# Kernel optimization log

Hardware: AMD Instinct MI355X
Metric: run time of the kernel (lower is better)

Reference implementation:

```python
import jax, jax.numpy as jnp
import numpy as np
import math

B, S, D = 2, 4096, 512
H = 8
DH = D // H  # 64


def setup_inputs() -> dict:
    key = jax.random.key(0)
    k1, k2, k3, k4, k5 = jax.random.split(key, 5)
    scale = 1.0 / math.sqrt(D)
    return {
        "x": jax.random.normal(k1, (B, S, D), dtype=jnp.float32),
        "W_in": jax.random.normal(k2, (D, 3 * D), dtype=jnp.float32) * scale,
        "b_in": jax.random.normal(k3, (3 * D,), dtype=jnp.float32) * 0.01,
        "W_out": jax.random.normal(k4, (D, D), dtype=jnp.float32) * scale,
        "b_out": jax.random.normal(k5, (D,), dtype=jnp.float32) * 0.01,
        "causal_mask": 1,
    }


def reference(x, W_in, b_in, W_out, b_out, causal_mask):
    b, s, d = x.shape
    # fused QKV projection: (b, s, 3d)
    qkv = x @ W_in + b_in
    q, k, v = jnp.split(qkv, 3, axis=-1)
    # (b, s, d) -> (b, h, s, dh)
    def to_heads(t):
        return t.reshape(b, s, H, DH).transpose(0, 2, 1, 3)
    q, k, v = to_heads(q), to_heads(k), to_heads(v)
    # raw scores (b, h, s, s)
    scores = jnp.einsum("bhqd,bhkd->bhqk", q, k)
    if causal_mask:  # static python flag
        # upper-triangular (strictly above diag) -> -inf, applied pre-scaling
        # (matches source; -inf invariant under /sqrt(d_head))
        tri = jnp.triu(jnp.ones((s, s), dtype=bool), k=1)
        scores = jnp.where(tri, -jnp.inf, scores)
    attn = jax.nn.softmax(scores / math.sqrt(DH), axis=-1)
    out = jnp.einsum("bhqk,bhkd->bhqd", attn, v)
    out = out.transpose(0, 2, 1, 3).reshape(b, s, d)
    return out @ W_out + b_out
```

## Files before the change

### kernel.cpp

```cpp
#include <hip/hip_runtime.h>
#include <cstdint>
#include <cmath>

typedef unsigned short BF16;
typedef __attribute__((ext_vector_type(8))) short short8;
typedef __attribute__((ext_vector_type(4))) float f32x4;
typedef __attribute__((ext_vector_type(16))) float f32x16;
typedef __attribute__((ext_vector_type(2))) unsigned int uint2v;
typedef __attribute__((ext_vector_type(4))) unsigned int uint4v;

#define S_LEN 4096
#define DMODEL 512
#define NHEAD 8
#define DHEAD 64
#define BS 2
#define NROWS (BS * NHEAD * S_LEN)

__device__ __forceinline__ BF16 f2bf(float f) {
  union { float f; uint32_t u; } v; v.f = f;
  uint32_t r = (v.u + 0x7FFFu + ((v.u >> 16) & 1u)) >> 16;
  return (BF16)r;
}

__device__ __forceinline__ unsigned cvtpk(float a, float b) {
  unsigned r;
  asm volatile("v_cvt_pk_bf16_f32 %0, %1, %2" : "=v"(r) : "v"(a), "v"(b));
  return r;
}

__device__ __forceinline__ float partner32(float x, int hi) {
  unsigned a = __float_as_uint(x), b = a;
  uint2v r = __builtin_amdgcn_permlane32_swap(a, b, false, false);
  return __uint_as_float(hi ? r[0] : r[1]);
}

__device__ __forceinline__ void pl32(unsigned &a, unsigned &b) {
  uint2v r = __builtin_amdgcn_permlane32_swap(a, b, false, false);
  a = r[0]; b = r[1];
}

__device__ __forceinline__ void gload16(const void* g, void* lds) {
  __builtin_amdgcn_global_load_lds(
      (const __attribute__((address_space(1))) void*)g,
      (__attribute__((address_space(3))) void*)lds, 16, 0, 0);
}

#define MAX3(a, b, c) fmaxf(fmaxf((a), (b)), (c))
#define CS_CONST 0.18033688011112042f

__global__ __launch_bounds__(256) void cvt_x_k(const float* __restrict__ x,
                                               BF16* __restrict__ xb) {
  int i = blockIdx.x * 256 + threadIdx.x;
  float4 v = reinterpret_cast<const float4*>(x)[i];
  ushort4 o;
  o.x = f2bf(v.x); o.y = f2bf(v.y); o.z = f2bf(v.z); o.w = f2bf(v.w);
  reinterpret_cast<ushort4*>(xb)[i] = o;
}

__global__ __launch_bounds__(256) void tr_cvt_k(const float* __restrict__ W,
                                                BF16* __restrict__ Wt,
                                                int K, int N) {
  __shared__ float t[32][33];
  int n0 = blockIdx.x * 32, k0 = blockIdx.y * 32;
  int tx = threadIdx.x & 31, ty = threadIdx.x >> 5;
#pragma unroll
  for (int i = 0; i < 4; ++i)
    t[ty + 8 * i][tx] = W[(size_t)(k0 + ty + 8 * i) * N + n0 + tx];
  __syncthreads();
#pragma unroll
  for (int i = 0; i < 4; ++i)
    Wt[(size_t)(n0 + ty + 8 * i) * K + k0 + tx] = f2bf(t[tx][ty + 8 * i]);
}

template <int MODE>
__global__ __launch_bounds__(256)
void gemm_k(const BF16* __restrict__ A, const BF16* __restrict__ Bt,
            const float* __restrict__ bias,
            BF16* __restrict__ Qb, BF16* __restrict__ Kb, BF16* __restrict__ Vt,
            float* __restrict__ Out) {
  __shared__ BF16 As[128 * 64];
  __shared__ BF16 Bs[128 * 64];
  const int tid = threadIdx.x;
  const int l = tid & 63, w = tid >> 6;
  const int wm = w >> 1, wn = w & 1;
  const int bm = blockIdx.x, bn = blockIdx.y;
  f32x4 acc[4][4] = {};

  for (int kt = 0; kt < 512 / 64; ++kt) {
#pragma unroll
    for (int i = 0; i < 4; ++i) {
      int ldsoff = i * 4096 + w * 1024;
      int off = ldsoff + l * 16;
      int row = off >> 7;
      int slot = ((off >> 4) & 7) ^ (row & 7);
      gload16(A + (size_t)(bm * 128 + row) * 512 + kt * 64 + slot * 8,
              (char*)As + ldsoff);
      gload16(Bt + (size_t)(bn * 128 + row) * 512 + kt * 64 + slot * 8,
              (char*)Bs + ldsoff);
    }
    __syncthreads();
    const char* Ab = (const char*)As;
    const char* Bb = (const char*)Bs;
    short8 af[4][2], bfr[4][2];
#pragma unroll
    for (int mf = 0; mf < 4; ++mf)
#pragma unroll
      for (int kk = 0; kk < 2; ++kk) {
        int row = wm * 64 + mf * 16 + (l & 15);
        int slot = ((l >> 4) + 4 * kk) ^ (row & 7);
        af[mf][kk] = *(const short8*)(Ab + row * 128 + slot * 16);
      }
#pragma unroll
    for (int nf = 0; nf < 4; ++nf)
#pragma unroll
      for (int kk = 0; kk < 2; ++kk) {
        int row = wn * 64 + nf * 16 + (l & 15);
        int slot = ((l >> 4) + 4 * kk) ^ (row & 7);
        bfr[nf][kk] = *(const short8*)(Bb + row * 128 + slot * 16);
      }
    __builtin_amdgcn_s_setprio(1);
#pragma unroll
    for (int kk = 0; kk < 2; ++kk)
#pragma unroll
      for (int mf = 0; mf < 4; ++mf)
#pragma unroll
        for (int nf = 0; nf < 4; ++nf)
          acc[mf][nf] = __builtin_amdgcn_mfma_f32_16x16x32_bf16(
              af[mf][kk], bfr[nf][kk], acc[mf][nf], 0, 0, 0);
    __builtin_amdgcn_s_setprio(0);
    __syncthreads();
  }

#pragma unroll
  for (int mf = 0; mf < 4; ++mf)
#pragma unroll
    for (int nf = 0; nf < 4; ++nf)
#pragma unroll
      for (int r = 0; r < 4; ++r) {
        int row = bm * 128 + wm * 64 + mf * 16 + ((l >> 4) << 2) + r;
        int col = bn * 128 + wn * 64 + nf * 16 + (l & 15);
        float v = acc[mf][nf][r] + bias[col];
        if (MODE == 0) {
          int sec = col >> 9, nl = col & 511;
          int h = nl >> 6, dh = nl & 63;
          int b = row >> 12, s = row & 4095;
          size_t bh = (size_t)(b * NHEAD + h);
          if (sec == 0)
            Qb[(bh * S_LEN + s) * DHEAD + dh] = f2bf(v);
          else if (sec == 1)
            Kb[(bh * S_LEN + s) * DHEAD + dh] = f2bf(v);
          else
            Vt[(bh * DHEAD + dh) * S_LEN + s] = f2bf(v);
        } else {
          Out[(size_t)row * DMODEL + col] = v;
        }
      }
}

__global__ __launch_bounds__(256, 4)
void attn_k(const BF16* __restrict__ Qg, const BF16* __restrict__ Kg,
            const BF16* __restrict__ Vg, BF16* __restrict__ Opb,
            float* __restrict__ Ml) {
  __shared__ BF16 Kl[2][64 * 64];
  __shared__ BF16 Vl[2][64 * 64];
  const int tid = threadIdx.x, l = tid & 63, w = tid >> 6;
  const int hi = l >> 5, ln = l & 31;
  const int wgid = blockIdx.x;
  const int xcd = wgid & 7, j = wgid >> 3;
  const int bh = xcd * 2 + (j & 1);
  const int qr = (j >> 1) & 3;
  const int p = j >> 3;
  const BF16* Qh = Qg + (size_t)bh * S_LEN * DHEAD;
  const BF16* Kh = Kg + (size_t)bh * S_LEN * DHEAD;
  const BF16* Vh = Vg + (size_t)bh * DHEAD * S_LEN;
  const float CS = CS_CONST;

  int cur = 0;
  for (int rep = 0; rep < 2; ++rep) {
    const int qt = rep ? (31 - p) : p;
    const int qq = rep ? (3 - qr) : qr;
    const int NTf = 2 * qt + 2;
    const int kbase = (qq * NTf) >> 2;
    const int kend = ((qq + 1) * NTf) >> 2;
    const int NT = kend - kbase;
    const int q0w = qt * 128 + w * 32;
    const int qrow = q0w + ln;
    __syncthreads();

    short8 qb[4];
    {
      const BF16* qp = Qh + (size_t)qrow * DHEAD + hi * 8;
#pragma unroll
      for (int ks = 0; ks < 4; ++ks) qb[ks] = *(const short8*)(qp + ks * 16);
    }
    f32x16 oacc0 = {}, oacc1 = {};
    float m_ = -INFINITY, l_ = 0.f;

    auto stage = [&](int buf, int ktile) {
      const int kv0 = ktile * 64;
#pragma unroll
      for (int i = 0; i < 2; ++i) {
        int base = i * 4096 + w * 1024;
        int off = base + l * 16;
        int row = off >> 7;
        int slot = ((off >> 4) & 7) ^ (row & 7);
        gload16(Kh + (size_t)(kv0 + row) * DHEAD + slot * 8, (char*)Kl[buf] + base);
        gload16(Vh + (size_t)row * S_LEN + kv0 + slot * 8, (char*)Vl[buf] + base);
      }
    };

    if (NT > 0) {
      stage(cur, kbase);
      for (int kt = 0; kt < NT; ++kt) {
        __syncthreads();
        if (kt + 1 < NT) stage(cur ^ 1, kbase + kt + 1);
        const int kv0 = (kbase + kt) * 64;
        if (kv0 <= q0w + 31) {
          const char* Kb_ = (const char*)Kl[cur];
          f32x16 s0 = {}, s1 = {};
          __builtin_amdgcn_s_setprio(1);
#pragma unroll
          for (int ks = 0; ks < 4; ++ks) {
            int slot0 = (2 * ks + hi) ^ (ln & 7);
            short8 kf0 = *(const short8*)(Kb_ + ln * 128 + slot0 * 16);
            int row1 = 32 + ln;
            int slot1 = (2 * ks + hi) ^ (row1 & 7);
            short8 kf1 = *(const short8*)(Kb_ + row1 * 128 + slot1 * 16);
            s0 = __builtin_amdgcn_mfma_f32_32x32x16_bf16(kf0, qb[ks], s0, 0, 0, 0);
            s1 = __builtin_amdgcn_mfma_f32_32x32x16_bf16(kf1, qb[ks], s1, 0, 0, 0);
          }
          __builtin_amdgcn_s_setprio(0);
          if (kv0 + 63 > q0w) {
#pragma unroll
            for (int r = 0; r < 16; ++r) {
              int crow = (r & 3) + 8 * (r >> 2) + 4 * hi;
              if (kv0 + crow > qrow) s0[r] = -INFINITY;
              if (kv0 + 32 + crow > qrow) s1[r] = -INFINITY;
            }
          }
          float a0 = MAX3(s0[0], s0[1], s0[2]);
          float a1 = MAX3(s0[3], s0[4], s0[5]);
          float a2 = MAX3(s0[6], s0[7], s0[8]);
          float a3 = MAX3(s0[9], s0[10], s0[11]);
          float a4 = MAX3(s0[12], s0[13], s0[14]);
          float a5 = MAX3(s0[15], s1[0], s1[1]);
          float a6 = MAX3(s1[2], s1[3], s1[4]);
          float a7 = MAX3(s1[5], s1[6], s1[7]);
          float a8 = MAX3(s1[8], s1[9], s1[10]);
          float a9 = MAX3(s1[11], s1[12], s1[13]);
          float a10 = fmaxf(s1[14], s1[15]);
          float b0 = MAX3(a0, a1, a2);
          float b1 = MAX3(a3, a4, a5);
          float b2 = MAX3(a6, a7, a8);
          float b3 = fmaxf(a9, a10);
          float pmax = fmaxf(fmaxf(b0, b1), fmaxf(b2, b3));
          pmax = fmaxf(pmax, partner32(pmax, hi));
          bool need = (pmax - m_) * CS > 8.0f;
          if (__any(need)) {
            float mn = fmaxf(m_, pmax);
            float alpha = exp2f((m_ - mn) * CS);
            m_ = mn;
            l_ *= alpha;
#pragma unroll
            for (int r = 0; r < 16; ++r) { oacc0[r] *= alpha; oacc1[r] *= alpha; }
          }
          const float mb = m_ * CS;
          float p0[16], p1[16];
          float rs = 0.f;
#pragma unroll
          for (int r = 0; r < 16; ++r) { p0[r] = exp2f(fmaf(s0[r], CS, -mb)); rs += p0[r]; }
#pragma unroll
          for (int r = 0; r < 16; ++r) { p1[r] = exp2f(fmaf(s1[r], CS, -mb)); rs += p1[r]; }
          rs += partner32(rs, hi);
          l_ += rs;
          short8 pf[4];
#pragma unroll
          for (int hf = 0; hf < 2; ++hf) {
            const float* pp = hf ? p1 : p0;
            unsigned w01 = cvtpk(pp[0], pp[1]), w23 = cvtpk(pp[2], pp[3]);
            unsigned w45 = cvtpk(pp[4], pp[5]), w67 = cvtpk(pp[6], pp[7]);
            unsigned w89 = cvtpk(pp[8], pp[9]), wab = cvtpk(pp[10], pp[11]);
            unsigned wcd = cvtpk(pp[12], pp[13]), wef = cvtpk(pp[14], pp[15]);
            pl32(w01, w45);
            pl32(w23, w67);
            pl32(w89, wcd);
            pl32(wab, wef);
            union { uint4v u; short8 s; } c0, c1;
            c0.u = (uint4v){w01, w23, w45, w67};
            c1.u = (uint4v){w89, wab, wcd, wef};
            pf[hf * 2 + 0] = c0.s;
            pf[hf * 2 + 1] = c1.s;
          }
          const char* Vb_ = (const char*)Vl[cur];
          __builtin_amdgcn_s_setprio(1);
#pragma unroll
          for (int ks = 0; ks < 4; ++ks) {
            int slot0 = (2 * ks + hi) ^ (ln & 7);
            short8 vf0 = *(const short8*)(Vb_ + ln * 128 + slot0 * 16);
            int row1 = 32 + ln;
            int slot1 = (2 * ks + hi) ^ (row1 & 7);
            short8 vf1 = *(const short8*)(Vb_ + row1 * 128 + slot1 * 16);
            oacc0 = __builtin_amdgcn_mfma_f32_32x32x16_bf16(vf0, pf[ks], oacc0, 0, 0, 0);
            oacc1 = __builtin_amdgcn_mfma_f32_32x32x16_bf16(vf1, pf[ks], oacc1, 0, 0, 0);
          }
          __builtin_amdgcn_s_setprio(0);
        }
        cur ^= 1;
      }
    }

    BF16* Op = Opb + ((size_t)qq * NROWS + (size_t)bh * S_LEN + qrow) * DHEAD;
#pragma unroll
    for (int blk = 0; blk < 2; ++blk) {
      const f32x16 oa = blk ? oacc1 : oacc0;
#pragma unroll
      for (int g = 0; g < 4; ++g) {
        int dh0 = 8 * g + 4 * hi + 32 * blk;
        unsigned lo = cvtpk(oa[4 * g + 0], oa[4 * g + 1]);
        unsigned h2 = cvtpk(oa[4 * g + 2], oa[4 * g + 3]);
        uint2v st = {lo, h2};
        *(uint2v*)(Op + dh0) = st;
      }
    }
    if (hi == 0) {
      float2 ml = {m_, l_};
      *(float2*)(Ml + ((size_t)qq * NROWS + (size_t)bh * S_LEN + qrow) * 2) = ml;
    }
  }
}

__global__ __launch_bounds__(256)
void merge_k(const BF16* __restrict__ Opb, const float* __restrict__ Ml,
             BF16* __restrict__ Ob) {
  const int wv = blockIdx.x * 4 + (threadIdx.x >> 6);
  const int lane = threadIdx.x & 63;
  const int row0 = wv * 64;
  for (int r = 0; r < 64; ++r) {
    int row = row0 + r;
    float2 ml0 = *(const float2*)(Ml + (size_t)row * 2);
    float2 ml1 = *(const float2*)(Ml + ((size_t)NROWS + row) * 2);
    float2 ml2 = *(const float2*)(Ml + ((size_t)2 * NROWS + row) * 2);
    float2 ml3 = *(const float2*)(Ml + ((size_t)3 * NROWS + row) * 2);
    float m = fmaxf(fmaxf(ml0.x, ml1.x), fmaxf(ml2.x, ml3.x));
    float a0 = exp2f((ml0.x - m) * CS_CONST);
    float a1 = exp2f((ml1.x - m) * CS_CONST);
    float a2 = exp2f((ml2.x - m) * CS_CONST);
    float a3 = exp2f((ml3.x - m) * CS_CONST);
    float linv = 1.0f / (ml0.y * a0 + ml1.y * a1 + ml2.y * a2 + ml3.y * a3);
    union { unsigned short u; } t;
    auto ld = [&](int slot) -> float {
      unsigned short u = Opb[((size_t)slot * NROWS + row) * DHEAD + lane];
      unsigned x = ((unsigned)u) << 16;
      return __uint_as_float(x);
    };
    float o = (ld(0) * a0 + ld(1) * a1 + ld(2) * a2 + ld(3) * a3) * linv;
    (void)t;
    int bh = row >> 12, s = row & 4095;
    Ob[((size_t)((bh >> 3) * S_LEN + s)) * DMODEL + (bh & 7) * DHEAD + lane] = f2bf(o);
  }
}

extern "C" void kernel_launch(void* const* d_in, const int* in_sizes, int n_in,
                              void* d_out, int out_size, void* d_ws, size_t ws_size,
                              hipStream_t stream) {
  const float* x = (const float*)d_in[0];
  const float* W_in = (const float*)d_in[1];
  const float* b_in = (const float*)d_in[2];
  const float* W_out = (const float*)d_in[3];
  const float* b_out = (const float*)d_in[4];
  float* out = (float*)d_out;

  char* ws = (char*)d_ws;
  const size_t SZ_X = (size_t)BS * S_LEN * DMODEL * 2;
  const size_t SZ_OP = (size_t)NROWS * DHEAD * 2;
  BF16* xb    = (BF16*)(ws);
  BF16* wint  = (BF16*)(ws + SZ_X);
  BF16* woutt = (BF16*)(ws + SZ_X + 3 * DMODEL * DMODEL * 2);
  BF16* Qb    = (BF16*)(ws + SZ_X + 4 * DMODEL * DMODEL * 2);
  BF16* Kb    = (BF16*)((char*)Qb + SZ_X);
  BF16* Vt    = (BF16*)((char*)Kb + SZ_X);
  BF16* Ob    = (BF16*)((char*)Vt + SZ_X);
  BF16* Opb   = (BF16*)((char*)Ob + SZ_X);
  float* Ml   = (float*)((char*)Opb + 4 * SZ_OP);

  cvt_x_k<<<dim3((BS * S_LEN * DMODEL) / 4 / 256), 256, 0, stream>>>(x, xb);
  tr_cvt_k<<<dim3(3 * DMODEL / 32, DMODEL / 32), 256, 0, stream>>>(W_in, wint, DMODEL, 3 * DMODEL);
  tr_cvt_k<<<dim3(DMODEL / 32, DMODEL / 32), 256, 0, stream>>>(W_out, woutt, DMODEL, DMODEL);
  gemm_k<0><<<dim3(BS * S_LEN / 128, 3 * DMODEL / 128), 256, 0, stream>>>(
      xb, wint, b_in, Qb, Kb, Vt, nullptr);
  attn_k<<<dim3(1024), 256, 0, stream>>>(Qb, Kb, Vt, Opb, Ml);
  merge_k<<<dim3(256), 256, 0, stream>>>(Opb, Ml, Ob);
  gemm_k<1><<<dim3(BS * S_LEN / 128, DMODEL / 128), 256, 0, stream>>>(
      Ob, woutt, b_out, nullptr, nullptr, nullptr, out);
}
```

Before: 215.1 us.

## Merge weight transposes, add separate V transpose, MFMA row sums, vectorize merge

Several unrelated changes. The two weight-transpose launches become one kernel. The QKV GEMM now writes V in the same row-major layout as Q and K, and a new LDS-tiled kernel transposes it into the reused x buffer, which avoids the strided scattered V stores. Inside attention, the softmax row-sum reduction and its cross-lane permute are replaced by an extra MFMA against a ones vector, trading VALU work for matrix-core work. The merge kernel is vectorized to 8 bf16 per lane with packed stores and twice as many blocks. The extra launch and the third MFMA per step are the costs.

```diff
diff --git a/kernel.cpp b/kernel.cpp
--- a/kernel.cpp
+++ b/kernel.cpp
@@ -20,6 +20,10 @@
   union { float f; uint32_t u; } v; v.f = f;
   uint32_t r = (v.u + 0x7FFFu + ((v.u >> 16) & 1u)) >> 16;
   return (BF16)r;
+}
+
+__device__ __forceinline__ float bf2f(short u) {
+  return __uint_as_float(((unsigned)(unsigned short)u) << 16);
 }
 
 __device__ __forceinline__ unsigned cvtpk(float a, float b) {
@@ -57,11 +61,18 @@
   reinterpret_cast<ushort4*>(xb)[i] = o;
 }
 
-__global__ __launch_bounds__(256) void tr_cvt_k(const float* __restrict__ W,
-                                                BF16* __restrict__ Wt,
-                                                int K, int N) {
+__global__ __launch_bounds__(256) void trw_k(const float* __restrict__ W_in,
+                                             const float* __restrict__ W_out,
+                                             BF16* __restrict__ wint,
+                                             BF16* __restrict__ woutt) {
   __shared__ float t[32][33];
-  int n0 = blockIdx.x * 32, k0 = blockIdx.y * 32;
+  const bool second = blockIdx.x >= 48;
+  const float* W = second ? W_out : W_in;
+  BF16* Wt = second ? woutt : wint;
+  const int N = second ? DMODEL : 3 * DMODEL;
+  const int K = DMODEL;
+  int n0 = (second ? ((int)blockIdx.x - 48) : (int)blockIdx.x) * 32;
+  int k0 = blockIdx.y * 32;
   int tx = threadIdx.x & 31, ty = threadIdx.x >> 5;
 #pragma unroll
   for (int i = 0; i < 4; ++i)
@@ -76,7 +87,7 @@
 __global__ __launch_bounds__(256)
 void gemm_k(const BF16* __restrict__ A, const BF16* __restrict__ Bt,
             const float* __restrict__ bias,
-            BF16* __restrict__ Qb, BF16* __restrict__ Kb, BF16* __restrict__ Vt,
+            BF16* __restrict__ Qb, BF16* __restrict__ Kb, BF16* __restrict__ Vc,
             float* __restrict__ Out) {
   __shared__ BF16 As[128 * 64];
   __shared__ BF16 Bs[128 * 64];
@@ -144,17 +155,36 @@
           int sec = col >> 9, nl = col & 511;
           int h = nl >> 6, dh = nl & 63;
           int b = row >> 12, s = row & 4095;
-          size_t bh = (size_t)(b * NHEAD + h);
-          if (sec == 0)
-            Qb[(bh * S_LEN + s) * DHEAD + dh] = f2bf(v);
-          else if (sec == 1)
-            Kb[(bh * S_LEN + s) * DHEAD + dh] = f2bf(v);
-          else
-            Vt[(bh * DHEAD + dh) * S_LEN + s] = f2bf(v);
+          BF16* dst = sec == 0 ? Qb : (sec == 1 ? Kb : Vc);
+          dst[(((size_t)(b * NHEAD + h)) * S_LEN + s) * DHEAD + dh] = f2bf(v);
         } else {
           Out[(size_t)row * DMODEL + col] = v;
         }
       }
+}
+
+__global__ __launch_bounds__(256)
+void v_tr_k(const BF16* __restrict__ Vc, BF16* __restrict__ Vt) {
+  __shared__ BF16 t[64][66];
+  const int bh = blockIdx.y, st = blockIdx.x;
+  const int tid = threadIdx.x;
+  const int g = tid >> 3, c8 = (tid & 7) * 8;
+#pragma unroll
+  for (int p = 0; p < 2; ++p) {
+    int s = p * 32 + g;
+    short8 v = *(const short8*)(Vc + ((size_t)bh * S_LEN + st * 64 + s) * DHEAD + c8);
+#pragma unroll
+    for (int j = 0; j < 8; ++j) t[s][c8 + j] = (BF16)(unsigned short)v[j];
+  }
+  __syncthreads();
+#pragma unroll
+  for (int p = 0; p < 2; ++p) {
+    int dh = p * 32 + g;
+    short8 o;
+#pragma unroll
+    for (int j = 0; j < 8; ++j) o[j] = (short)t[c8 + j][dh];
+    *(short8*)(Vt + ((size_t)bh * DHEAD + dh) * S_LEN + st * 64 + c8) = o;
+  }
 }
 
 __global__ __launch_bounds__(256, 4)
@@ -174,6 +204,9 @@
   const BF16* Kh = Kg + (size_t)bh * S_LEN * DHEAD;
   const BF16* Vh = Vg + (size_t)bh * DHEAD * S_LEN;
   const float CS = CS_CONST;
+  short8 ones;
+#pragma unroll
+  for (int i = 0; i < 8; ++i) ones[i] = (short)0x3F80;
 
   int cur = 0;
   for (int rep = 0; rep < 2; ++rep) {
@@ -193,8 +226,8 @@
 #pragma unroll
       for (int ks = 0; ks < 4; ++ks) qb[ks] = *(const short8*)(qp + ks * 16);
     }
-    f32x16 oacc0 = {}, oacc1 = {};
-    float m_ = -INFINITY, l_ = 0.f;
+    f32x16 oacc0 = {}, oacc1 = {}, lacc = {};
+    float m_ = -INFINITY;
 
     auto stage = [&](int buf, int ktile) {
       const int kv0 = ktile * 64;
@@ -260,19 +293,16 @@
             float mn = fmaxf(m_, pmax);
             float alpha = exp2f((m_ - mn) * CS);
             m_ = mn;
-            l_ *= alpha;
+            lacc[0] *= alpha;
 #pragma unroll
             for (int r = 0; r < 16; ++r) { oacc0[r] *= alpha; oacc1[r] *= alpha; }
           }
           const float mb = m_ * CS;
           float p0[16], p1[16];
-          float rs = 0.f;
-#pragma unroll
-          for (int r = 0; r < 16; ++r) { p0[r] = exp2f(fmaf(s0[r], CS, -mb)); rs += p0[r]; }
-#pragma unroll
-          for (int r = 0; r < 16; ++r) { p1[r] = exp2f(fmaf(s1[r], CS, -mb)); rs += p1[r]; }
-          rs += partner32(rs, hi);
-          l_ += rs;
+#pragma unroll
+          for (int r = 0; r < 16; ++r) p0[r] = exp2f(fmaf(s0[r], CS, -mb));
+#pragma unroll
+          for (int r = 0; r < 16; ++r) p1[r] = exp2f(fmaf(s1[r], CS, -mb));
           short8 pf[4];
 #pragma unroll
           for (int hf = 0; hf < 2; ++hf) {
@@ -302,6 +332,7 @@
             short8 vf1 = *(const short8*)(Vb_ + row1 * 128 + slot1 * 16);
             oacc0 = __builtin_amdgcn_mfma_f32_32x32x16_bf16(vf0, pf[ks], oacc0, 0, 0, 0);
             oacc1 = __builtin_amdgcn_mfma_f32_32x32x16_bf16(vf1, pf[ks], oacc1, 0, 0, 0);
+            lacc = __builtin_amdgcn_mfma_f32_32x32x16_bf16(ones, pf[ks], lacc, 0, 0, 0);
           }
           __builtin_amdgcn_s_setprio(0);
         }
@@ -323,7 +354,7 @@
       }
     }
     if (hi == 0) {
-      float2 ml = {m_, l_};
+      float2 ml = {m_, lacc[0]};
       *(float2*)(Ml + ((size_t)qq * NROWS + (size_t)bh * S_LEN + qrow) * 2) = ml;
     }
   }
@@ -334,9 +365,10 @@
              BF16* __restrict__ Ob) {
   const int wv = blockIdx.x * 4 + (threadIdx.x >> 6);
   const int lane = threadIdx.x & 63;
-  const int row0 = wv * 64;
-  for (int r = 0; r < 64; ++r) {
-    int row = row0 + r;
+  const int r_off = lane >> 3, c8 = (lane & 7) * 8;
+#pragma unroll
+  for (int it = 0; it < 4; ++it) {
+    int row = wv * 32 + it * 8 + r_off;
     float2 ml0 = *(const float2*)(Ml + (size_t)row * 2);
     float2 ml1 = *(const float2*)(Ml + ((size_t)NROWS + row) * 2);
     float2 ml2 = *(const float2*)(Ml + ((size_t)2 * NROWS + row) * 2);
@@ -347,16 +379,21 @@
     float a2 = exp2f((ml2.x - m) * CS_CONST);
     float a3 = exp2f((ml3.x - m) * CS_CONST);
     float linv = 1.0f / (ml0.y * a0 + ml1.y * a1 + ml2.y * a2 + ml3.y * a3);
-    union { unsigned short u; } t;
-    auto ld = [&](int slot) -> float {
-      unsigned short u = Opb[((size_t)slot * NROWS + row) * DHEAD + lane];
-      unsigned x = ((unsigned)u) << 16;
-      return __uint_as_float(x);
-    };
-    float o = (ld(0) * a0 + ld(1) * a1 + ld(2) * a2 + ld(3) * a3) * linv;
-    (void)t;
+    a0 *= linv; a1 *= linv; a2 *= linv; a3 *= linv;
+    short8 v0 = *(const short8*)(Opb + ((size_t)0 * NROWS + row) * DHEAD + c8);
+    short8 v1 = *(const short8*)(Opb + ((size_t)1 * NROWS + row) * DHEAD + c8);
+    short8 v2 = *(const short8*)(Opb + ((size_t)2 * NROWS + row) * DHEAD + c8);
+    short8 v3 = *(const short8*)(Opb + ((size_t)3 * NROWS + row) * DHEAD + c8);
+    float o[8];
+#pragma unroll
+    for (int jj = 0; jj < 8; ++jj)
+      o[jj] = bf2f(v0[jj]) * a0 + bf2f(v1[jj]) * a1 +
+              bf2f(v2[jj]) * a2 + bf2f(v3[jj]) * a3;
+    uint4v pk = {cvtpk(o[0], o[1]), cvtpk(o[2], o[3]),
+                 cvtpk(o[4], o[5]), cvtpk(o[6], o[7])};
     int bh = row >> 12, s = row & 4095;
-    Ob[((size_t)((bh >> 3) * S_LEN + s)) * DMODEL + (bh & 7) * DHEAD + lane] = f2bf(o);
+    *(uint4v*)(Ob + ((size_t)((bh >> 3) * S_LEN + s)) * DMODEL +
+               (bh & 7) * DHEAD + c8) = pk;
   }
 }
 
@@ -374,22 +411,23 @@
   const size_t SZ_X = (size_t)BS * S_LEN * DMODEL * 2;
   const size_t SZ_OP = (size_t)NROWS * DHEAD * 2;
   BF16* xb    = (BF16*)(ws);
+  BF16* Vt    = xb;
   BF16* wint  = (BF16*)(ws + SZ_X);
   BF16* woutt = (BF16*)(ws + SZ_X + 3 * DMODEL * DMODEL * 2);
   BF16* Qb    = (BF16*)(ws + SZ_X + 4 * DMODEL * DMODEL * 2);
   BF16* Kb    = (BF16*)((char*)Qb + SZ_X);
-  BF16* Vt    = (BF16*)((char*)Kb + SZ_X);
-  BF16* Ob    = (BF16*)((char*)Vt + SZ_X);
+  BF16* Vc    = (BF16*)((char*)Kb + SZ_X);
+  BF16* Ob    = (BF16*)((char*)Vc + SZ_X);
   BF16* Opb   = (BF16*)((char*)Ob + SZ_X);
   float* Ml   = (float*)((char*)Opb + 4 * SZ_OP);
 
   cvt_x_k<<<dim3((BS * S_LEN * DMODEL) / 4 / 256), 256, 0, stream>>>(x, xb);
-  tr_cvt_k<<<dim3(3 * DMODEL / 32, DMODEL / 32), 256, 0, stream>>>(W_in, wint, DMODEL, 3 * DMODEL);
-  tr_cvt_k<<<dim3(DMODEL / 32, DMODEL / 32), 256, 0, stream>>>(W_out, woutt, DMODEL, DMODEL);
+  trw_k<<<dim3(64, DMODEL / 32), 256, 0, stream>>>(W_in, W_out, wint, woutt);
   gemm_k<0><<<dim3(BS * S_LEN / 128, 3 * DMODEL / 128), 256, 0, stream>>>(
-      xb, wint, b_in, Qb, Kb, Vt, nullptr);
+      xb, wint, b_in, Qb, Kb, Vc, nullptr);
+  v_tr_k<<<dim3(S_LEN / 64, BS * NHEAD), 256, 0, stream>>>(Vc, Vt);
   attn_k<<<dim3(1024), 256, 0, stream>>>(Qb, Kb, Vt, Opb, Ml);
-  merge_k<<<dim3(256), 256, 0, stream>>>(Opb, Ml, Ob);
+  merge_k<<<dim3(512), 256, 0, stream>>>(Opb, Ml, Ob);
   gemm_k<1><<<dim3(BS * S_LEN / 128, DMODEL / 128), 256, 0, stream>>>(
       Ob, woutt, b_out, nullptr, nullptr, nullptr, out);
 }
```

New measurement: 201.6 us. -6.3%, faster.
